# Optimization experiments

Hardware: AMD Instinct MI355X
Metric: run time of the kernel (lower is better)

## Reference

```python
import jax, jax.numpy as jnp
import numpy as np

N = 8192      # nodes
D_IN = 128    # input features
D_H = 48      # GAT hidden (hardcoded in module)
D_OUT = 32    # control output dim
NEG_INF = -9e15  # matches torch code's -9000000000000000.0


def setup_inputs() -> dict:
    key = jax.random.key(0)
    ks = jax.random.split(key, 12)
    s = 0.05
    return {
        "x": jax.random.normal(ks[0], (N, D_IN), jnp.float32),
        "adj": jax.random.randint(ks[1], (N, N), 0, 2, jnp.int32),
        "W_gat": jax.random.normal(ks[2], (D_H, D_IN), jnp.float32) * s,
        "a": jax.random.normal(ks[3], (1, D_H), jnp.float32) * s,
        "gamma": jnp.ones((D_H,), jnp.float32),
        "beta": jnp.zeros((D_H,), jnp.float32),
        "W1": jax.random.normal(ks[4], (256, D_H), jnp.float32) * s,
        "b1": jnp.zeros((256,), jnp.float32),
        "W2": jax.random.normal(ks[5], (128, 256), jnp.float32) * s,
        "b2": jnp.zeros((128,), jnp.float32),
        "W3": jax.random.normal(ks[6], (D_OUT, 128), jnp.float32) * s,
        "b3": jnp.zeros((D_OUT,), jnp.float32),
    }


def reference(x, adj, W_gat, a, gamma, beta, W1, b1, W2, b2, W3, b3):
    # --- LightweightGATLayer ---
    Wh = x @ W_gat.T                      # [N, D_H]
    s = Wh @ a.T                          # [N, 1] additive attention scores
    e = s + s.T                           # [N, N]
    e = jnp.where(e > 0, e, 0.2 * e)      # LeakyReLU(0.2)
    e = jnp.where(adj > 0, e, NEG_INF)    # mask non-edges
    attn = jax.nn.softmax(e, axis=1)      # row softmax; dropout is identity in eval
    h_prime = attn @ Wh                   # [N, D_H]
    # LayerNorm over last dim, eps=1e-5
    mu = jnp.mean(h_prime, axis=-1, keepdims=True)
    var = jnp.var(h_prime, axis=-1, keepdims=True)
    h = (h_prime - mu) * jax.lax.rsqrt(var + 1e-5) * gamma + beta
    # --- BiACT MLP head: 48 -> 256 -> 128 -> D_OUT ---
    h = jax.nn.relu(h @ W1.T + b1)
    h = jax.nn.relu(h @ W2.T + b2)
    return h @ W3.T + b3                  # [N, D_OUT]
```

## Files before the change

kernel.cpp:

```cpp
#include <hip/hip_runtime.h>

#define N 8192
#define DIN 128
#define DH 48
#define MT 256
#define KC 64
#define PSTR (MT + 4)
#define ACC_STRIDE 52
#define RB 32

__global__ __launch_bounds__(256) void k_wh(const float* __restrict__ x,
                                            const float* __restrict__ Wg,
                                            float* __restrict__ Wh) {
    __shared__ float wT[DIN * DH];
    int t = threadIdx.x;
    for (int e = t; e < DIN * DH; e += 256) {
        int c = e / DIN, k = e % DIN;
        wT[k * DH + c] = Wg[e];
    }
    __syncthreads();
    int o = blockIdx.x * 256 + t;
    int r = o / DH, c = o % DH;
    const float4* xr = (const float4*)(x + (size_t)r * DIN);
    float acc = 0.f;
    #pragma unroll 8
    for (int k4 = 0; k4 < DIN / 4; ++k4) {
        float4 xv = xr[k4];
        int kb = k4 * 4;
        acc += xv.x * wT[(kb + 0) * DH + c];
        acc += xv.y * wT[(kb + 1) * DH + c];
        acc += xv.z * wT[(kb + 2) * DH + c];
        acc += xv.w * wT[(kb + 3) * DH + c];
    }
    Wh[o] = acc;
}

__global__ __launch_bounds__(256) void k_s(const float* __restrict__ Wh,
                                           const float* __restrict__ a,
                                           float* __restrict__ s) {
    int r = blockIdx.x * 256 + threadIdx.x;
    const float4* wr = (const float4*)(Wh + (size_t)r * DH);
    const float4* av = (const float4*)a;
    float acc = 0.f;
    #pragma unroll
    for (int k4 = 0; k4 < DH / 4; ++k4) {
        float4 w = wr[k4]; float4 aa = av[k4];
        acc += w.x * aa.x + w.y * aa.y + w.z * aa.z + w.w * aa.w;
    }
    s[r] = acc;
}

__global__ __launch_bounds__(256) void k_gat(const int* __restrict__ adj,
                                             const float* __restrict__ Wh,
                                             const float* __restrict__ s,
                                             float* __restrict__ accWs,
                                             int jspan, int nchunk) {
    __shared__ float pT[KC][PSTR];
    __shared__ float wS[KC][DH];
    __shared__ float sRow[MT];
    int t = threadIdx.x;
    int tile = blockIdx.x & 31;
    int split = blockIdx.x >> 5;
    int i0 = tile * MT;
    int jbase = split * jspan;

    int lane = t & 63;
    int w = t >> 6;

    sRow[t] = s[i0 + t];

    float acc[4][12];
    #pragma unroll
    for (int rr = 0; rr < 4; ++rr)
        #pragma unroll
        for (int d = 0; d < 12; ++d) acc[rr][d] = 0.f;
    float lsum[4] = {0.f, 0.f, 0.f, 0.f};

    __syncthreads();

    for (int chunk = 0; chunk < nchunk; ++chunk) {
        int j0 = jbase + chunk * KC;
        {
            const float4* wsrc = (const float4*)(Wh + (size_t)j0 * DH);
            float4* wdst = (float4*)&wS[0][0];
            #pragma unroll
            for (int k = 0; k < 3; ++k) wdst[t + k * 256] = wsrc[t + k * 256];
        }
        {
            int j = j0 + lane;
            float sj = s[j];
            #pragma unroll 4
            for (int it = 0; it < 16; ++it) {
                int r0 = (w * 16 + it) * 4;
                float4 pv;
                #pragma unroll
                for (int k = 0; k < 4; ++k) {
                    int av = adj[(size_t)(i0 + r0 + k) * N + j];
                    float e = sRow[r0 + k] + sj;
                    e = fmaxf(e, 0.2f * e);
                    ((float*)&pv)[k] = (av > 0) ? __expf(e) : 0.f;
                }
                *(float4*)&pT[lane][r0] = pv;
            }
        }
        __syncthreads();
        {
            const int rbase = lane * 4;
            const int dbase = w * 12;
            #pragma unroll 4
            for (int jj = 0; jj < KC; ++jj) {
                float4 p = *(const float4*)&pT[jj][rbase];
                const float4* wr = (const float4*)&wS[jj][dbase];
                float4 w0 = wr[0], w1 = wr[1], w2 = wr[2];
                #pragma unroll
                for (int rr = 0; rr < 4; ++rr) {
                    float pr = ((const float*)&p)[rr];
                    acc[rr][0] += pr * w0.x; acc[rr][1]  += pr * w0.y;
                    acc[rr][2] += pr * w0.z; acc[rr][3]  += pr * w0.w;
                    acc[rr][4] += pr * w1.x; acc[rr][5]  += pr * w1.y;
                    acc[rr][6] += pr * w1.z; acc[rr][7]  += pr * w1.w;
                    acc[rr][8] += pr * w2.x; acc[rr][9]  += pr * w2.y;
                    acc[rr][10] += pr * w2.z; acc[rr][11] += pr * w2.w;
                }
                if (w == 0) {
                    #pragma unroll
                    for (int rr = 0; rr < 4; ++rr)
                        lsum[rr] += ((const float*)&p)[rr];
                }
            }
        }
        __syncthreads();
    }
    size_t base = (size_t)split * N + i0 + lane * 4;
    #pragma unroll
    for (int rr = 0; rr < 4; ++rr) {
        float* orow = accWs + (base + rr) * ACC_STRIDE + w * 12;
        ((float4*)orow)[0] = make_float4(acc[rr][0], acc[rr][1], acc[rr][2], acc[rr][3]);
        ((float4*)orow)[1] = make_float4(acc[rr][4], acc[rr][5], acc[rr][6], acc[rr][7]);
        ((float4*)orow)[2] = make_float4(acc[rr][8], acc[rr][9], acc[rr][10], acc[rr][11]);
        if (w == 0)
            accWs[(base + rr) * ACC_STRIDE + 48] = lsum[rr];
    }
}

__global__ __launch_bounds__(256) void k_mlp(const float* __restrict__ accWs,
                                             const float* __restrict__ gamma,
                                             const float* __restrict__ beta,
                                             const float* __restrict__ W1, const float* __restrict__ b1,
                                             const float* __restrict__ W2, const float* __restrict__ b2,
                                             const float* __restrict__ W3, const float* __restrict__ b3,
                                             float* __restrict__ out, int nsplit) {
    __shared__ float hacc[RB * 49];
    __shared__ float hN[RB * DH];
    __shared__ float h1[RB * 256];
    __shared__ float h2[RB * 128];
    int t = threadIdx.x;
    int r0 = blockIdx.x * RB;

    for (int e = t; e < RB * 49; e += 256) {
        int r = e / 49, d = e % 49;
        size_t base = (size_t)(r0 + r) * ACC_STRIDE + d;
        float v = 0.f;
        for (int sp = 0; sp < nsplit; ++sp)
            v += accWs[(size_t)sp * N * ACC_STRIDE + base];
        hacc[r * 49 + d] = v;
    }
    __syncthreads();

    if (t < RB) {
        float invl = 1.f / hacc[t * 49 + 48];
        float sum = 0.f;
        for (int d = 0; d < DH; ++d) sum += hacc[t * 49 + d];
        float mean = sum * invl * (1.f / DH);
        float var = 0.f;
        for (int d = 0; d < DH; ++d) {
            float dv = hacc[t * 49 + d] * invl - mean;
            var += dv * dv;
        }
        var *= (1.f / DH);
        float rs = rsqrtf(var + 1e-5f);
        for (int d = 0; d < DH; ++d) {
            float hv = (hacc[t * 49 + d] * invl - mean) * rs;
            hN[t * DH + d] = hv * gamma[d] + beta[d];
        }
    }
    __syncthreads();

    {
        int c = t;
        float4 wreg[12];
        const float4* wrow = (const float4*)(W1 + c * DH);
        #pragma unroll
        for (int k4 = 0; k4 < 12; ++k4) wreg[k4] = wrow[k4];
        float bias = b1[c];
        for (int r = 0; r < RB; ++r) {
            float acc = bias;
            const float4* hv4 = (const float4*)&hN[r * DH];
            #pragma unroll
            for (int k4 = 0; k4 < 12; ++k4) {
                float4 hv = hv4[k4];
                acc += hv.x * wreg[k4].x + hv.y * wreg[k4].y
                     + hv.z * wreg[k4].z + hv.w * wreg[k4].w;
            }
            h1[r * 256 + c] = fmaxf(acc, 0.f);
        }
    }
    __syncthreads();

    {
        int c = t & 127;
        int g = t >> 7;
        int rb = g * 16;
        float acc[16];
        float bias = b2[c];
        #pragma unroll
        for (int r = 0; r < 16; ++r) acc[r] = bias;
        const float4* wrow = (const float4*)(W2 + c * 256);
        for (int k4 = 0; k4 < 64; ++k4) {
            float4 wv = wrow[k4];
            #pragma unroll
            for (int r = 0; r < 16; ++r) {
                const float4 hv = *(const float4*)(&h1[(rb + r) * 256 + k4 * 4]);
                acc[r] += wv.x * hv.x + wv.y * hv.y + wv.z * hv.z + wv.w * hv.w;
            }
        }
        #pragma unroll
        for (int r = 0; r < 16; ++r)
            h2[(rb + r) * 128 + c] = fmaxf(acc[r], 0.f);
    }
    __syncthreads();

    {
        int c = t & 31;
        int g = t >> 5;
        int rb = g * 4;
        float acc[4];
        float bias = b3[c];
        #pragma unroll
        for (int r = 0; r < 4; ++r) acc[r] = bias;
        const float4* wrow = (const float4*)(W3 + c * 128);
        for (int k4 = 0; k4 < 32; ++k4) {
            float4 wv = wrow[k4];
            #pragma unroll
            for (int r = 0; r < 4; ++r) {
                const float4 hv = *(const float4*)(&h2[(rb + r) * 128 + k4 * 4]);
                acc[r] += wv.x * hv.x + wv.y * hv.y + wv.z * hv.z + wv.w * hv.w;
            }
        }
        #pragma unroll
        for (int r = 0; r < 4; ++r)
            out[(size_t)(r0 + rb + r) * 32 + c] = acc[r];
    }
}

extern "C" void kernel_launch(void* const* d_in, const int* in_sizes, int n_in,
                              void* d_out, int out_size, void* d_ws, size_t ws_size,
                              hipStream_t stream) {
    const float* x     = (const float*)d_in[0];
    const int*   adj   = (const int*)d_in[1];
    const float* Wg    = (const float*)d_in[2];
    const float* a     = (const float*)d_in[3];
    const float* gamma = (const float*)d_in[4];
    const float* beta  = (const float*)d_in[5];
    const float* W1    = (const float*)d_in[6];
    const float* b1    = (const float*)d_in[7];
    const float* W2    = (const float*)d_in[8];
    const float* b2    = (const float*)d_in[9];
    const float* W3    = (const float*)d_in[10];
    const float* b3    = (const float*)d_in[11];
    float* out = (float*)d_out;

    float* ws = (float*)d_ws;
    float* Wh    = ws;
    float* s     = ws + (size_t)N * DH;
    float* accWs = s + N;

    size_t avail = ws_size / 4 - ((size_t)N * DH + N);
    int nsplit = (avail >= (size_t)16 * N * ACC_STRIDE) ? 16 : 8;
    int jspan = N / nsplit;
    int nchunk = jspan / KC;

    k_wh<<<N * DH / 256, 256, 0, stream>>>(x, Wg, Wh);
    k_s<<<N / 256, 256, 0, stream>>>(Wh, a, s);
    k_gat<<<32 * nsplit, 256, 0, stream>>>(adj, Wh, s, accWs, jspan, nchunk);
    k_mlp<<<N / RB, 256, 0, stream>>>(accWs, gamma, beta, W1, b1, W2, b2, W3, b3, out, nsplit);
}
```

Measured before the change: 495.0 us.

## Use fp16 MFMA for GAT attention-weighted aggregation with ones-column row sums

Replaces the scalar FMA accumulation of exp-scores times Wh with 16x16x32 fp16 MFMA instructions. Probabilities and Wh are converted to half in shared memory, and an extra ones-column in the B tile yields the softmax denominators directly. Adjacency loads become int2-vectorized, and the split count is fixed at 16 regardless of available workspace. The risks are fp16 precision loss on unnormalized exp values, including possible overflow, and a larger workspace stride that assumes enough ws_size.

```diff
diff --git a/kernel.cpp b/kernel.cpp
--- a/kernel.cpp
+++ b/kernel.cpp
@@ -5,9 +5,15 @@
 #define DH 48
 #define MT 256
 #define KC 64
-#define PSTR (MT + 4)
-#define ACC_STRIDE 52
+#define PSTR (KC + 8)
+#define NSPLIT 16
+#define JSPAN (N / NSPLIT)
+#define NCHUNK (JSPAN / KC)
+#define ACC_STRIDE 64
 #define RB 32
+
+typedef _Float16 half8 __attribute__((ext_vector_type(8)));
+typedef float f32x4 __attribute__((ext_vector_type(4)));
 
 __global__ __launch_bounds__(256) void k_wh(const float* __restrict__ x,
                                             const float* __restrict__ Wg,
@@ -53,93 +59,95 @@
 __global__ __launch_bounds__(256) void k_gat(const int* __restrict__ adj,
                                              const float* __restrict__ Wh,
                                              const float* __restrict__ s,
-                                             float* __restrict__ accWs,
-                                             int jspan, int nchunk) {
-    __shared__ float pT[KC][PSTR];
-    __shared__ float wS[KC][DH];
+                                             float* __restrict__ accWs) {
+    __shared__ _Float16 pS[MT][PSTR];
+    __shared__ _Float16 wS[64][PSTR];
     __shared__ float sRow[MT];
     int t = threadIdx.x;
     int tile = blockIdx.x & 31;
     int split = blockIdx.x >> 5;
     int i0 = tile * MT;
-    int jbase = split * jspan;
-
-    int lane = t & 63;
-    int w = t >> 6;
+    int jbase = split * JSPAN;
 
     sRow[t] = s[i0 + t];
-
-    float acc[4][12];
+    for (int e = t; e < 16 * PSTR; e += 256) {
+        int n = 48 + e / PSTR, k = e % PSTR;
+        wS[n][k] = (n == 48) ? (_Float16)1.0f : (_Float16)0.0f;
+    }
+
+    int lane = t & 63, w = t >> 6;
+    int ln16 = lane & 15, kq = lane >> 4;
+    int jp = t & 31, rg = t >> 5;
+
+    f32x4 acc[4][4];
     #pragma unroll
-    for (int rr = 0; rr < 4; ++rr)
-        #pragma unroll
-        for (int d = 0; d < 12; ++d) acc[rr][d] = 0.f;
-    float lsum[4] = {0.f, 0.f, 0.f, 0.f};
-
-    __syncthreads();
-
-    for (int chunk = 0; chunk < nchunk; ++chunk) {
+    for (int a0 = 0; a0 < 4; ++a0)
+        #pragma unroll
+        for (int b0 = 0; b0 < 4; ++b0) acc[a0][b0] = (f32x4){0.f, 0.f, 0.f, 0.f};
+
+    __syncthreads();
+
+    for (int chunk = 0; chunk < NCHUNK; ++chunk) {
         int j0 = jbase + chunk * KC;
+        #pragma unroll
+        for (int k = 0; k < 12; ++k) {
+            int e = t + k * 256;
+            int jc = e / DH, d = e % DH;
+            wS[d][jc] = (_Float16)Wh[(size_t)j0 * DH + e];
+        }
         {
-            const float4* wsrc = (const float4*)(Wh + (size_t)j0 * DH);
-            float4* wdst = (float4*)&wS[0][0];
-            #pragma unroll
-            for (int k = 0; k < 3; ++k) wdst[t + k * 256] = wsrc[t + k * 256];
-        }
-        {
-            int j = j0 + lane;
-            float sj = s[j];
-            #pragma unroll 4
-            for (int it = 0; it < 16; ++it) {
-                int r0 = (w * 16 + it) * 4;
-                float4 pv;
-                #pragma unroll
-                for (int k = 0; k < 4; ++k) {
-                    int av = adj[(size_t)(i0 + r0 + k) * N + j];
-                    float e = sRow[r0 + k] + sj;
-                    e = fmaxf(e, 0.2f * e);
-                    ((float*)&pv)[k] = (av > 0) ? __expf(e) : 0.f;
-                }
-                *(float4*)&pT[lane][r0] = pv;
+            float2 sj = *(const float2*)(s + j0 + 2 * jp);
+            #pragma unroll 8
+            for (int it = 0; it < 32; ++it) {
+                int r = rg * 32 + it;
+                int2 av = *(const int2*)(adj + (size_t)(i0 + r) * N + j0 + 2 * jp);
+                float e0 = sRow[r] + sj.x;
+                float e1 = sRow[r] + sj.y;
+                e0 = fmaxf(e0, 0.2f * e0);
+                e1 = fmaxf(e1, 0.2f * e1);
+                float p0 = av.x ? __expf(e0) : 0.f;
+                float p1 = av.y ? __expf(e1) : 0.f;
+                union { _Float16 h[2]; unsigned u; } pk;
+                pk.h[0] = (_Float16)p0;
+                pk.h[1] = (_Float16)p1;
+                *(unsigned*)&pS[r][2 * jp] = pk.u;
             }
         }
         __syncthreads();
         {
-            const int rbase = lane * 4;
-            const int dbase = w * 12;
-            #pragma unroll 4
-            for (int jj = 0; jj < KC; ++jj) {
-                float4 p = *(const float4*)&pT[jj][rbase];
-                const float4* wr = (const float4*)&wS[jj][dbase];
-                float4 w0 = wr[0], w1 = wr[1], w2 = wr[2];
+            const int m0 = w * 64;
+            #pragma unroll
+            for (int kt = 0; kt < 2; ++kt) {
+                const int kk = kt * 32 + kq * 8;
+                half8 b[4];
                 #pragma unroll
-                for (int rr = 0; rr < 4; ++rr) {
-                    float pr = ((const float*)&p)[rr];
-                    acc[rr][0] += pr * w0.x; acc[rr][1]  += pr * w0.y;
-                    acc[rr][2] += pr * w0.z; acc[rr][3]  += pr * w0.w;
-                    acc[rr][4] += pr * w1.x; acc[rr][5]  += pr * w1.y;
-                    acc[rr][6] += pr * w1.z; acc[rr][7]  += pr * w1.w;
-                    acc[rr][8] += pr * w2.x; acc[rr][9]  += pr * w2.y;
-                    acc[rr][10] += pr * w2.z; acc[rr][11] += pr * w2.w;
+                for (int nt = 0; nt < 4; ++nt)
+                    b[nt] = *(const half8*)&wS[nt * 16 + ln16][kk];
+                #pragma unroll
+                for (int mtl = 0; mtl < 4; ++mtl) {
+                    half8 a = *(const half8*)&pS[m0 + mtl * 16 + ln16][kk];
+                    #pragma unroll
+                    for (int nt = 0; nt < 4; ++nt)
+                        acc[mtl][nt] = __builtin_amdgcn_mfma_f32_16x16x32_f16(
+                            a, b[nt], acc[mtl][nt], 0, 0, 0);
                 }
-                if (w == 0) {
-                    #pragma unroll
-                    for (int rr = 0; rr < 4; ++rr)
-                        lsum[rr] += ((const float*)&p)[rr];
-                }
             }
         }
         __syncthreads();
     }
-    size_t base = (size_t)split * N + i0 + lane * 4;
+    size_t rbase = (size_t)split * N + i0;
     #pragma unroll
-    for (int rr = 0; rr < 4; ++rr) {
-        float* orow = accWs + (base + rr) * ACC_STRIDE + w * 12;
-        ((float4*)orow)[0] = make_float4(acc[rr][0], acc[rr][1], acc[rr][2], acc[rr][3]);
-        ((float4*)orow)[1] = make_float4(acc[rr][4], acc[rr][5], acc[rr][6], acc[rr][7]);
-        ((float4*)orow)[2] = make_float4(acc[rr][8], acc[rr][9], acc[rr][10], acc[rr][11]);
-        if (w == 0)
-            accWs[(base + rr) * ACC_STRIDE + 48] = lsum[rr];
+    for (int mtl = 0; mtl < 4; ++mtl) {
+        #pragma unroll
+        for (int nt = 0; nt < 4; ++nt) {
+            int col = nt * 16 + ln16;
+            if (nt == 3 && ln16 != 0) continue;
+            #pragma unroll
+            for (int reg = 0; reg < 4; ++reg) {
+                int row = w * 64 + mtl * 16 + kq * 4 + reg;
+                accWs[(rbase + row) * ACC_STRIDE + col] = acc[mtl][nt][reg];
+            }
+        }
     }
 }
 
@@ -149,7 +157,7 @@
                                              const float* __restrict__ W1, const float* __restrict__ b1,
                                              const float* __restrict__ W2, const float* __restrict__ b2,
                                              const float* __restrict__ W3, const float* __restrict__ b3,
-                                             float* __restrict__ out, int nsplit) {
+                                             float* __restrict__ out) {
     __shared__ float hacc[RB * 49];
     __shared__ float hN[RB * DH];
     __shared__ float h1[RB * 256];
@@ -161,7 +169,8 @@
         int r = e / 49, d = e % 49;
         size_t base = (size_t)(r0 + r) * ACC_STRIDE + d;
         float v = 0.f;
-        for (int sp = 0; sp < nsplit; ++sp)
+        #pragma unroll
+        for (int sp = 0; sp < NSPLIT; ++sp)
             v += accWs[(size_t)sp * N * ACC_STRIDE + base];
         hacc[r * 49 + d] = v;
     }
@@ -275,13 +284,8 @@
     float* s     = ws + (size_t)N * DH;
     float* accWs = s + N;
 
-    size_t avail = ws_size / 4 - ((size_t)N * DH + N);
-    int nsplit = (avail >= (size_t)16 * N * ACC_STRIDE) ? 16 : 8;
-    int jspan = N / nsplit;
-    int nchunk = jspan / KC;
-
     k_wh<<<N * DH / 256, 256, 0, stream>>>(x, Wg, Wh);
     k_s<<<N / 256, 256, 0, stream>>>(Wh, a, s);
-    k_gat<<<32 * nsplit, 256, 0, stream>>>(adj, Wh, s, accWs, jspan, nchunk);
-    k_mlp<<<N / RB, 256, 0, stream>>>(accWs, gamma, beta, W1, b1, W2, b2, W3, b3, out, nsplit);
-}
+    k_gat<<<32 * NSPLIT, 256, 0, stream>>>(adj, Wh, s, accWs);
+    k_mlp<<<N / RB, 256, 0, stream>>>(accWs, gamma, beta, W1, b1, W2, b2, W3, b3, out);
+}
```

After: 463.4 us. 1.07x faster.
